# Performance work log

Hardware: AMD Instinct MI355X
Metric: run time of the kernel (lower is better)

Reference implementation:

```python
import jax, jax.numpy as jnp
import numpy as np


def setup_inputs() -> dict:
    key = jax.random.key(0)
    ks = jax.random.split(key, 8)
    B, C, H, W = 4, 128, 64, 64
    C8 = C // 8
    return {
        "x": jax.random.normal(ks[0], (B, C, H, W), dtype=jnp.float32),
        "Wq": jax.random.normal(ks[1], (C8, C), dtype=jnp.float32) * (1.0 / np.sqrt(C)),
        "bq": jax.random.normal(ks[2], (C8,), dtype=jnp.float32) * 0.01,
        "Wk": jax.random.normal(ks[3], (C8, C), dtype=jnp.float32) * (1.0 / np.sqrt(C)),
        "bk": jax.random.normal(ks[4], (C8,), dtype=jnp.float32) * 0.01,
        "Wv": jax.random.normal(ks[5], (C, C), dtype=jnp.float32) * (1.0 / np.sqrt(C)),
        "bv": jax.random.normal(ks[6], (C,), dtype=jnp.float32) * 0.01,
        "gamma": jax.random.normal(ks[7], (1,), dtype=jnp.float32),
    }


def reference(x, Wq, bq, Wk, bk, Wv, bv, gamma):
    B, C, H, W = x.shape
    N = H * W
    xf = x.reshape(B, C, N)  # flatten spatial dims; 1x1 conv == channel matmul
    q = jnp.einsum("oc,bcn->bon", Wq, xf) + bq[None, :, None]  # (B, C8, N)
    k = jnp.einsum("oc,bcn->bon", Wk, xf) + bk[None, :, None]  # (B, C8, N)
    v = jnp.einsum("oc,bcn->bon", Wv, xf) + bv[None, :, None]  # (B, C, N)
    scores = jnp.einsum("bci,bcj->bij", q, k)  # (B, N, N), query rows x key cols
    attn = jax.nn.softmax(scores, axis=-1)
    out = jnp.einsum("bcj,bij->bci", v, attn)  # (B, C, N)
    out = out.reshape(B, C, H, W)
    return gamma[0] * out + x
```

## Files before the change

### kernel.cpp

```cpp
#include <hip/hip_runtime.h>
#include <math.h>

typedef __attribute__((ext_vector_type(8))) short bf16x8;
typedef __attribute__((ext_vector_type(16))) float f32x16;

constexpr int Bn = 4, Cn = 128, C8n = 16, Nn = 4096;

#if __has_builtin(__builtin_amdgcn_exp2f)
#define EXP2F(x) __builtin_amdgcn_exp2f(x)
#else
#define EXP2F(x) exp2f(x)
#endif

__device__ inline unsigned short f2bf(float f) {
    unsigned u = __builtin_bit_cast(unsigned, f);
    u += 0x7fff + ((u >> 16) & 1);
    return (unsigned short)(u >> 16);
}
__device__ inline unsigned pack2(float a, float b) {
    return (unsigned)f2bf(a) | ((unsigned)f2bf(b) << 16);
}
__device__ inline unsigned pkt(float a, float b) {
#if __has_builtin(__builtin_amdgcn_perm)
    return __builtin_amdgcn_perm(__builtin_bit_cast(unsigned, b),
                                 __builtin_bit_cast(unsigned, a), 0x07060302u);
#else
    return (__builtin_bit_cast(unsigned, a) >> 16) |
           (__builtin_bit_cast(unsigned, b) & 0xffff0000u);
#endif
}

__global__ __launch_bounds__(256) void qkv_kernel(
    const float* __restrict__ x,
    const float* __restrict__ Wq, const float* __restrict__ bq,
    const float* __restrict__ Wk, const float* __restrict__ bk,
    const float* __restrict__ Wv, const float* __restrict__ bv,
    unsigned short* __restrict__ qT, unsigned short* __restrict__ kT,
    unsigned short* __restrict__ vsw)
{
    __shared__ unsigned short wlds[96 * 128];
    __shared__ unsigned short v_s[64 * 64];
    __shared__ float qk_s[32][65];
    __shared__ float bfl[96];

    const int tid = threadIdx.x;
    const int b = blockIdx.x >> 6, n0 = (blockIdx.x & 63) << 6;
    const int y = blockIdx.y;
    const int w = tid >> 6, lane = tid & 63, col = lane & 31, half = lane >> 5;
    const int g01 = w >> 1;
    const float L2E = 1.4426950408889634f;
    const int RBASE = y ? 96 : 0;
    const int RCNT  = y ? 64 : 96;

    const int nx = n0 + ((w & 1) << 5);
    const float* xb = x + ((size_t)b * Cn) * Nn + nx + col;
    bf16x8 af[8];
    #pragma unroll
    for (int s = 0; s < 8; ++s) {
        float v[8];
        #pragma unroll
        for (int j = 0; j < 8; ++j)
            v[j] = xb[(size_t)(16 * s + 8 * half + j) * Nn];
        uint4 u = make_uint4(pack2(v[0], v[1]), pack2(v[2], v[3]),
                             pack2(v[4], v[5]), pack2(v[6], v[7]));
        af[s] = __builtin_bit_cast(bf16x8, u);
    }

    {
        unsigned* wl32 = (unsigned*)wlds;
        for (int i = tid; i < RCNT * 32; i += 256) {
            int rl = i >> 5, cq = (i & 31) << 2;
            int r = RBASE + rl;
            const float* src; float sc = 1.0f;
            if (r < 16)      { src = Wq + (size_t)r * Cn;        sc = L2E; }
            else if (r < 32) { src = Wk + (size_t)(r - 16) * Cn; }
            else             { src = Wv + (size_t)(r - 32) * Cn; }
            float4 t = *reinterpret_cast<const float4*>(&src[cq]);
            int G = cq >> 3;
            unsigned* wp = wl32 + 64 * rl + 4 * (G ^ (rl & 7)) + ((cq & 7) >> 1);
            wp[0] = pack2(t.x * sc, t.y * sc);
            wp[1] = pack2(t.z * sc, t.w * sc);
        }
        if (tid < RCNT) {
            int r = RBASE + tid;
            bfl[tid] = (r < 16) ? bq[r] * L2E
                     : (r < 32) ? bk[r - 16] : bv[r - 32];
        }
    }
    __syncthreads();

    const int mlA = (y == 0) ? (g01 ? 2 : 0) : g01;
    const bool hasB = (y == 0) && (g01 == 0);
    f32x16 a0, a1;
    {
        float b0 = bfl[32 * mlA + col];
        float b1 = hasB ? bfl[32 + col] : 0.0f;
        #pragma unroll
        for (int r = 0; r < 16; ++r) { a0[r] = b0; a1[r] = b1; }
    }
    #pragma unroll
    for (int s = 0; s < 8; ++s) {
        const int off = 8 * ((2 * s + half) ^ (col & 7));
        a0 = __builtin_amdgcn_mfma_f32_32x32x16_bf16(af[s],
             *(const bf16x8*)(wlds + 128 * (32 * mlA + col) + off), a0, 0, 0, 0);
        if (hasB)
            a1 = __builtin_amdgcn_mfma_f32_32x32x16_bf16(af[s],
                 *(const bf16x8*)(wlds + 128 * (32 + col) + off), a1, 0, 0, 0);
    }

    unsigned* vp32 = (unsigned*)v_s;
    #define VS_WRITE(A, C0) { \
        const int c_ = (C0) + col; \
        _Pragma("unroll") for (int g = 0; g < 4; ++g) { \
            int Gn = ((w & 1) << 2) + g; \
            unsigned* up = vp32 + 32 * c_ + 4 * (Gn ^ (c_ & 7)) + (half << 1); \
            up[0] = pack2(A[4 * g],     A[4 * g + 1]); \
            up[1] = pack2(A[4 * g + 2], A[4 * g + 3]); } }

    if (y == 0) {
        if (g01 == 0) {
            #pragma unroll
            for (int r = 0; r < 16; ++r)
                qk_s[col][((w & 1) << 5) + (r & 3) + ((r >> 2) << 3) + (half << 2)] = a0[r];
            VS_WRITE(a1, 0)
        } else {
            VS_WRITE(a0, 32)
        }
    } else {
        if (g01 == 0) { VS_WRITE(a0, 0)  }
        else          { VS_WRITE(a0, 32) }
    }
    #undef VS_WRITE
    __syncthreads();

    if (y == 0 && tid < 128) {
        int n = tid & 63, which = tid >> 6;
        unsigned wv_[8];
        #pragma unroll
        for (int i = 0; i < 8; ++i)
            wv_[i] = pack2(qk_s[16 * which + 2 * i][n], qk_s[16 * which + 2 * i + 1][n]);
        unsigned short* dst = (which ? kT : qT) + ((size_t)b * Nn + n0 + n) * C8n;
        *reinterpret_cast<uint4*>(dst)     = make_uint4(wv_[0], wv_[1], wv_[2], wv_[3]);
        *reinterpret_cast<uint4*>(dst + 8) = make_uint4(wv_[4], wv_[5], wv_[6], wv_[7]);
    }
    {
        const int ctl = w & 1, c_ = (ctl << 5) + col;
        const int tb = (w >> 1) << 1;
        #pragma unroll
        for (int tt = 0; tt < 2; ++tt) {
            int t = tb + tt;
            int Gn = (t << 1) + half;
            bf16x8 fr = *(const bf16x8*)(vp32 + 32 * c_ + 4 * (Gn ^ (c_ & 7)));
            size_t o_ = ((((size_t)b * 256 + (n0 >> 4) + t) * 4 + ((y << 1) | ctl)) * 64 + lane) * 8;
            *reinterpret_cast<uint4*>(&vsw[o_]) = __builtin_bit_cast(uint4, fr);
        }
    }
}

__global__ __launch_bounds__(512) void attn_kernel(
    const unsigned short* __restrict__ qT, const unsigned short* __restrict__ kT,
    const unsigned short* __restrict__ vsw, const float* __restrict__ x,
    const float* __restrict__ gamma_p, float* __restrict__ out)
{
    __shared__ unsigned sm_u32[8192];
    __shared__ float ls[2][2][64];
    __shared__ float invl[64];

    const int tid = threadIdx.x, wv = tid >> 6, lane = tid & 63;
    const int col = lane & 31, half = lane >> 5;
    const int xcd = blockIdx.x & 7;
    const int b = xcd >> 1;
    const int q0 = ((((blockIdx.x >> 3) << 1) | (xcd & 1))) << 6;

    const unsigned short* qb = qT + (size_t)b * Nn * C8n;
    bf16x8 qf0 = *(const bf16x8*)&qb[(size_t)(q0 + col) * C8n + 8 * half];
    bf16x8 qf1 = *(const bf16x8*)&qb[(size_t)(q0 + 32 + col) * C8n + 8 * half];

    f32x16 accA[4], accB[4];
    #pragma unroll
    for (int ct = 0; ct < 4; ++ct) { accA[ct] = {}; accB[ct] = {}; }
    float l0 = 0.0f, l1 = 0.0f;
    const unsigned short* kb = kT + (size_t)b * Nn * C8n;

#if __has_builtin(__builtin_amdgcn_permlane32_swap)
    #define MKPF(P, O, F) { \
        unsigned lo0 = pkt(P[O], P[O + 1]), lo1 = pkt(P[O + 2], P[O + 3]); \
        unsigned hi0 = pkt(P[O + 4], P[O + 5]), hi1 = pkt(P[O + 6], P[O + 7]); \
        auto r0 = __builtin_amdgcn_permlane32_swap(lo0, hi0, false, false); \
        auto r1 = __builtin_amdgcn_permlane32_swap(lo1, hi1, false, false); \
        uint4 u_ = make_uint4(r0[0], r1[0], r0[1], r1[1]); \
        F = __builtin_bit_cast(bf16x8, u_); }
#else
    #define MKPF(P, O, F) { \
        unsigned lo0 = pkt(P[O], P[O + 1]), lo1 = pkt(P[O + 2], P[O + 3]); \
        unsigned hi0 = pkt(P[O + 4], P[O + 5]), hi1 = pkt(P[O + 6], P[O + 7]); \
        unsigned t0 = half ? lo0 : hi0, t1 = half ? lo1 : hi1; \
        unsigned r0 = (unsigned)__shfl_xor((int)t0, 32); \
        unsigned r1 = (unsigned)__shfl_xor((int)t1, 32); \
        uint4 u_ = make_uint4(half ? r0 : lo0, half ? r1 : lo1, \
                              half ? hi0 : r0, half ? hi1 : r1); \
        F = __builtin_bit_cast(bf16x8, u_); }
#endif

    bf16x8 kf = *(const bf16x8*)&kb[(size_t)((wv << 9) + col) * C8n + 8 * half];

    #pragma unroll 1
    for (int kt = 0; kt < 16; ++kt) {
        const int j0 = (wv << 9) + (kt << 5);
        const int j0n = (wv << 9) + (((kt + 1) & 15) << 5);
        bf16x8 kf_next = *(const bf16x8*)&kb[(size_t)(j0n + col) * C8n + 8 * half];
        const size_t vbase = ((((size_t)b * 256 + (j0 >> 4)) * 4) * 64 + lane) * 8;
        bf16x8 va[4], vb2[4];
        #pragma unroll
        for (int ct = 0; ct < 4; ++ct) {
            va[ct]  = *(const bf16x8*)&vsw[vbase + (size_t)ct * 512];
            vb2[ct] = *(const bf16x8*)&vsw[vbase + (size_t)(4 + ct) * 512];
        }
        f32x16 z = {};

        {
            f32x16 s = __builtin_amdgcn_mfma_f32_32x32x16_bf16(kf, qf0, z, 0, 0, 0);
            float p[16]; float ps = 0.0f;
            #pragma unroll
            for (int r = 0; r < 16; ++r) { p[r] = EXP2F(s[r]); ps += p[r]; }
            l0 += ps;
            bf16x8 pf0, pf1;
            MKPF(p, 0, pf0) MKPF(p, 8, pf1)
            __builtin_amdgcn_s_setprio(1);
            #pragma unroll
            for (int ct = 0; ct < 4; ++ct) {
                accA[ct] = __builtin_amdgcn_mfma_f32_32x32x16_bf16(va[ct],  pf0, accA[ct], 0, 0, 0);
                accA[ct] = __builtin_amdgcn_mfma_f32_32x32x16_bf16(vb2[ct], pf1, accA[ct], 0, 0, 0);
            }
            __builtin_amdgcn_s_setprio(0);
        }
        {
            f32x16 s = __builtin_amdgcn_mfma_f32_32x32x16_bf16(kf, qf1, z, 0, 0, 0);
            float p[16]; float ps = 0.0f;
            #pragma unroll
            for (int r = 0; r < 16; ++r) { p[r] = EXP2F(s[r]); ps += p[r]; }
            l1 += ps;
            bf16x8 pf0, pf1;
            MKPF(p, 0, pf0) MKPF(p, 8, pf1)
            __builtin_amdgcn_s_setprio(1);
            #pragma unroll
            for (int ct = 0; ct < 4; ++ct) {
                accB[ct] = __builtin_amdgcn_mfma_f32_32x32x16_bf16(va[ct],  pf0, accB[ct], 0, 0, 0);
                accB[ct] = __builtin_amdgcn_mfma_f32_32x32x16_bf16(vb2[ct], pf1, accB[ct], 0, 0, 0);
            }
            __builtin_amdgcn_s_setprio(0);
        }
        kf = kf_next;
    }
    #undef MKPF

    l0 += __shfl_xor(l0, 32);
    l1 += __shfl_xor(l1, 32);

    #define SL_STORE(SL) { \
        ls[SL][0][lane] = l0; ls[SL][1][lane] = l1; \
        unsigned* sb = sm_u32 + (SL) * 4096; \
        _Pragma("unroll") for (int ct = 0; ct < 4; ++ct) \
        _Pragma("unroll") for (int i = 0; i < 8; ++i) { \
            sb[((ct) * 8 + i) * 64 + lane]     = pkt(accA[ct][2 * i], accA[ct][2 * i + 1]); \
            sb[((4 + ct) * 8 + i) * 64 + lane] = pkt(accB[ct][2 * i], accB[ct][2 * i + 1]); } }
    #define SL_ADD(SL) { \
        l0 += ls[SL][0][lane]; l1 += ls[SL][1][lane]; \
        unsigned* sb = sm_u32 + (SL) * 4096; \
        _Pragma("unroll") for (int ct = 0; ct < 4; ++ct) \
        _Pragma("unroll") for (int i = 0; i < 8; ++i) { \
            unsigned ua = sb[((ct) * 8 + i) * 64 + lane]; \
            accA[ct][2 * i]     += __builtin_bit_cast(float, ua << 16); \
            accA[ct][2 * i + 1] += __builtin_bit_cast(float, ua & 0xffff0000u); \
            unsigned ub = sb[((4 + ct) * 8 + i) * 64 + lane]; \
            accB[ct][2 * i]     += __builtin_bit_cast(float, ub << 16); \
            accB[ct][2 * i + 1] += __builtin_bit_cast(float, ub & 0xffff0000u); } }
    #define SL_RMW(SL) { \
        ls[SL][0][lane] += l0; ls[SL][1][lane] += l1; \
        unsigned* sb = sm_u32 + (SL) * 4096; \
        _Pragma("unroll") for (int ct = 0; ct < 4; ++ct) \
        _Pragma("unroll") for (int i = 0; i < 8; ++i) { \
            unsigned ua = sb[((ct) * 8 + i) * 64 + lane]; \
            float x0 = __builtin_bit_cast(float, ua << 16) + accA[ct][2 * i]; \
            float x1 = __builtin_bit_cast(float, ua & 0xffff0000u) + accA[ct][2 * i + 1]; \
            sb[((ct) * 8 + i) * 64 + lane] = pkt(x0, x1); \
            unsigned ub = sb[((4 + ct) * 8 + i) * 64 + lane]; \
            float y0 = __builtin_bit_cast(float, ub << 16) + accB[ct][2 * i]; \
            float y1 = __builtin_bit_cast(float, ub & 0xffff0000u) + accB[ct][2 * i + 1]; \
            sb[((4 + ct) * 8 + i) * 64 + lane] = pkt(y0, y1); } }

    if (wv == 4 || wv == 5) SL_STORE(wv - 4)
    __syncthreads();
    if (wv == 0 || wv == 1) SL_ADD(wv)
    __syncthreads();
    if (wv == 6 || wv == 7) SL_STORE(wv - 6)
    __syncthreads();
    if (wv == 2 || wv == 3) SL_RMW(wv - 2)
    __syncthreads();
    if (wv == 0 || wv == 1) SL_ADD(wv)
    __syncthreads();
    if (wv == 1) SL_STORE(0)
    __syncthreads();
    float* sf = (float*)sm_u32;
    if (wv == 0) {
        SL_ADD(0)
        #pragma unroll
        for (int ct = 0; ct < 4; ++ct)
            #pragma unroll
            for (int r = 0; r < 16; ++r) {
                sf[((ct) * 16 + r) * 64 + lane]     = accA[ct][r];
                sf[((4 + ct) * 16 + r) * 64 + lane] = accB[ct][r];
            }
        if (lane < 32) { invl[col] = 1.0f / l0; invl[32 + col] = 1.0f / l1; }
    }
    __syncthreads();
    #undef SL_STORE
    #undef SL_ADD
    #undef SL_RMW

    {
        const float g = gamma_p[0];
        const int n = tid & 63, ci = tid >> 6;
        const float il = invl[n];
        const int qs = n >> 5, nc = n & 31;
        #pragma unroll
        for (int p = 0; p < 16; ++p) {
            int ch = (p << 3) + ci;
            int ct = ch >> 5, chl = ch & 31;
            int h = (chl >> 2) & 1, r = (chl & 3) | ((chl >> 3) << 2);
            float val = sf[((qs * 4 + ct) * 16 + r) * 64 + nc + (h << 5)];
            size_t idx = ((size_t)(b * Cn + ch)) * Nn + q0 + n;
            out[idx] = g * (val * il) + x[idx];
        }
    }
}

extern "C" void kernel_launch(void* const* d_in, const int* in_sizes, int n_in,
                              void* d_out, int out_size, void* d_ws, size_t ws_size,
                              hipStream_t stream)
{
    const float* x     = (const float*)d_in[0];
    const float* Wq    = (const float*)d_in[1];
    const float* bq    = (const float*)d_in[2];
    const float* Wk    = (const float*)d_in[3];
    const float* bk    = (const float*)d_in[4];
    const float* Wv    = (const float*)d_in[5];
    const float* bv    = (const float*)d_in[6];
    const float* gamma = (const float*)d_in[7];
    float* out = (float*)d_out;

    unsigned short* ws16 = (unsigned short*)d_ws;
    unsigned short* qTw  = ws16;
    unsigned short* kTw  = qTw + (size_t)Bn * Nn * C8n;
    unsigned short* vsww = kTw + (size_t)Bn * Nn * C8n;

    qkv_kernel<<<dim3(256, 2), dim3(256), 0, stream>>>(
        x, Wq, bq, Wk, bk, Wv, bv, qTw, kTw, vsww);

    attn_kernel<<<dim3(256), dim3(512), 0, stream>>>(
        qTw, kTw, vsww, x, gamma, out);
}
```

Baseline: 107.7 us.

## Double-buffer V tile loads in attention loop and stage x through LDS

The attention main loop now prefetches the next iteration's V fragments together with the K fragment, using ping-pong register buffers (unrolled by two), so global V loads overlap the current MFMA/exp work. The QKV kernel loads the x tile with coalesced float4 reads into shared memory, then builds bf16 fragments from LDS instead of doing strided scalar global loads. This costs more VGPRs in the attention kernel, which may reduce occupancy, and adds 32KB of LDS in the QKV kernel.

```diff
diff --git a/kernel.cpp b/kernel.cpp
--- a/kernel.cpp
+++ b/kernel.cpp
@@ -38,6 +38,7 @@
     unsigned short* __restrict__ qT, unsigned short* __restrict__ kT,
     unsigned short* __restrict__ vsw)
 {
+    __shared__ float xs[Cn][64];
     __shared__ unsigned short wlds[96 * 128];
     __shared__ unsigned short v_s[64 * 64];
     __shared__ float qk_s[32][65];
@@ -52,18 +53,15 @@
     const int RBASE = y ? 96 : 0;
     const int RCNT  = y ? 64 : 96;
 
-    const int nx = n0 + ((w & 1) << 5);
-    const float* xb = x + ((size_t)b * Cn) * Nn + nx + col;
-    bf16x8 af[8];
-    #pragma unroll
-    for (int s = 0; s < 8; ++s) {
-        float v[8];
-        #pragma unroll
-        for (int j = 0; j < 8; ++j)
-            v[j] = xb[(size_t)(16 * s + 8 * half + j) * Nn];
-        uint4 u = make_uint4(pack2(v[0], v[1]), pack2(v[2], v[3]),
-                             pack2(v[4], v[5]), pack2(v[6], v[7]));
-        af[s] = __builtin_bit_cast(bf16x8, u);
+    {
+        const float* xb = x + ((size_t)b * Cn) * Nn + n0;
+        #pragma unroll
+        for (int k = 0; k < 8; ++k) {
+            int i = (k << 8) + tid;
+            int c = i >> 4, f4 = i & 15;
+            float4 t = *reinterpret_cast<const float4*>(&xb[(size_t)c * Nn + (f4 << 2)]);
+            *reinterpret_cast<float4*>(&xs[c][f4 << 2]) = t;
+        }
     }
 
     {
@@ -89,6 +87,19 @@
     }
     __syncthreads();
 
+    const int nloc = ((w & 1) << 5) + col;
+    bf16x8 af[8];
+    #pragma unroll
+    for (int s = 0; s < 8; ++s) {
+        const int cb = (s << 4) + (half << 3);
+        float v[8];
+        #pragma unroll
+        for (int j = 0; j < 8; ++j) v[j] = xs[cb + j][nloc];
+        uint4 u = make_uint4(pack2(v[0], v[1]), pack2(v[2], v[3]),
+                             pack2(v[4], v[5]), pack2(v[6], v[7]));
+        af[s] = __builtin_bit_cast(bf16x8, u);
+    }
+
     const int mlA = (y == 0) ? (g01 ? 2 : 0) : g01;
     const bool hasB = (y == 0) && (g01 == 0);
     f32x16 a0, a1;
@@ -181,6 +192,7 @@
     for (int ct = 0; ct < 4; ++ct) { accA[ct] = {}; accB[ct] = {}; }
     float l0 = 0.0f, l1 = 0.0f;
     const unsigned short* kb = kT + (size_t)b * Nn * C8n;
+    const f32x16 z = {};
 
 #if __has_builtin(__builtin_amdgcn_permlane32_swap)
     #define MKPF(P, O, F) { \
@@ -202,56 +214,58 @@
         F = __builtin_bit_cast(bf16x8, u_); }
 #endif
 
-    bf16x8 kf = *(const bf16x8*)&kb[(size_t)((wv << 9) + col) * C8n + 8 * half];
+    bf16x8 kfA, kfB, vxA[8], vxB[8];
+    {
+        kfA = *(const bf16x8*)&kb[(size_t)((wv << 9) + col) * C8n + 8 * half];
+        const size_t vb0 = ((((size_t)b * 256 + (wv << 5)) * 4) * 64 + lane) * 8;
+        #pragma unroll
+        for (int i = 0; i < 8; ++i)
+            vxA[i] = *(const bf16x8*)&vsw[vb0 + (size_t)i * 512];
+    }
+
+    #define ITER(KT, KC, VC, KN, VN) { \
+        const int ktn = ((KT) + 1) & 15; \
+        const int j0n = (wv << 9) + (ktn << 5); \
+        KN = *(const bf16x8*)&kb[(size_t)(j0n + col) * C8n + 8 * half]; \
+        const size_t vbn = ((((size_t)b * 256 + (j0n >> 4)) * 4) * 64 + lane) * 8; \
+        _Pragma("unroll") for (int i = 0; i < 8; ++i) \
+            VN[i] = *(const bf16x8*)&vsw[vbn + (size_t)i * 512]; \
+        { \
+            f32x16 s = __builtin_amdgcn_mfma_f32_32x32x16_bf16(KC, qf0, z, 0, 0, 0); \
+            float p[16]; float ps = 0.0f; \
+            _Pragma("unroll") for (int r = 0; r < 16; ++r) { p[r] = EXP2F(s[r]); ps += p[r]; } \
+            l0 += ps; \
+            bf16x8 pf0, pf1; \
+            MKPF(p, 0, pf0) MKPF(p, 8, pf1) \
+            __builtin_amdgcn_s_setprio(1); \
+            _Pragma("unroll") for (int ct = 0; ct < 4; ++ct) { \
+                accA[ct] = __builtin_amdgcn_mfma_f32_32x32x16_bf16(VC[ct],     pf0, accA[ct], 0, 0, 0); \
+                accA[ct] = __builtin_amdgcn_mfma_f32_32x32x16_bf16(VC[4 + ct], pf1, accA[ct], 0, 0, 0); \
+            } \
+            __builtin_amdgcn_s_setprio(0); \
+        } \
+        { \
+            f32x16 s = __builtin_amdgcn_mfma_f32_32x32x16_bf16(KC, qf1, z, 0, 0, 0); \
+            float p[16]; float ps = 0.0f; \
+            _Pragma("unroll") for (int r = 0; r < 16; ++r) { p[r] = EXP2F(s[r]); ps += p[r]; } \
+            l1 += ps; \
+            bf16x8 pf0, pf1; \
+            MKPF(p, 0, pf0) MKPF(p, 8, pf1) \
+            __builtin_amdgcn_s_setprio(1); \
+            _Pragma("unroll") for (int ct = 0; ct < 4; ++ct) { \
+                accB[ct] = __builtin_amdgcn_mfma_f32_32x32x16_bf16(VC[ct],     pf0, accB[ct], 0, 0, 0); \
+                accB[ct] = __builtin_amdgcn_mfma_f32_32x32x16_bf16(VC[4 + ct], pf1, accB[ct], 0, 0, 0); \
+            } \
+            __builtin_amdgcn_s_setprio(0); \
+        } }
 
     #pragma unroll 1
-    for (int kt = 0; kt < 16; ++kt) {
-        const int j0 = (wv << 9) + (kt << 5);
-        const int j0n = (wv << 9) + (((kt + 1) & 15) << 5);
-        bf16x8 kf_next = *(const bf16x8*)&kb[(size_t)(j0n + col) * C8n + 8 * half];
-        const size_t vbase = ((((size_t)b * 256 + (j0 >> 4)) * 4) * 64 + lane) * 8;
-        bf16x8 va[4], vb2[4];
-        #pragma unroll
-        for (int ct = 0; ct < 4; ++ct) {
-            va[ct]  = *(const bf16x8*)&vsw[vbase + (size_t)ct * 512];
-            vb2[ct] = *(const bf16x8*)&vsw[vbase + (size_t)(4 + ct) * 512];
-        }
-        f32x16 z = {};
-
-        {
-            f32x16 s = __builtin_amdgcn_mfma_f32_32x32x16_bf16(kf, qf0, z, 0, 0, 0);
-            float p[16]; float ps = 0.0f;
-            #pragma unroll
-            for (int r = 0; r < 16; ++r) { p[r] = EXP2F(s[r]); ps += p[r]; }
-            l0 += ps;
-            bf16x8 pf0, pf1;
-            MKPF(p, 0, pf0) MKPF(p, 8, pf1)
-            __builtin_amdgcn_s_setprio(1);
-            #pragma unroll
-            for (int ct = 0; ct < 4; ++ct) {
-                accA[ct] = __builtin_amdgcn_mfma_f32_32x32x16_bf16(va[ct],  pf0, accA[ct], 0, 0, 0);
-                accA[ct] = __builtin_amdgcn_mfma_f32_32x32x16_bf16(vb2[ct], pf1, accA[ct], 0, 0, 0);
-            }
-            __builtin_amdgcn_s_setprio(0);
-        }
-        {
-            f32x16 s = __builtin_amdgcn_mfma_f32_32x32x16_bf16(kf, qf1, z, 0, 0, 0);
-            float p[16]; float ps = 0.0f;
-            #pragma unroll
-            for (int r = 0; r < 16; ++r) { p[r] = EXP2F(s[r]); ps += p[r]; }
-            l1 += ps;
-            bf16x8 pf0, pf1;
-            MKPF(p, 0, pf0) MKPF(p, 8, pf1)
-            __builtin_amdgcn_s_setprio(1);
-            #pragma unroll
-            for (int ct = 0; ct < 4; ++ct) {
-                accB[ct] = __builtin_amdgcn_mfma_f32_32x32x16_bf16(va[ct],  pf0, accB[ct], 0, 0, 0);
-                accB[ct] = __builtin_amdgcn_mfma_f32_32x32x16_bf16(vb2[ct], pf1, accB[ct], 0, 0, 0);
-            }
-            __builtin_amdgcn_s_setprio(0);
-        }
-        kf = kf_next;
-    }
+    for (int kt2 = 0; kt2 < 8; ++kt2) {
+        const int kt0 = kt2 << 1;
+        ITER(kt0,     kfA, vxA, kfB, vxB)
+        ITER(kt0 + 1, kfB, vxB, kfA, vxA)
+    }
+    #undef ITER
     #undef MKPF
 
     l0 += __shfl_xor(l0, 32);
```

Result: slower. 149.3 us (+38.6%).
